# Performance work log

Measured on AMD Instinct MI355X. Metric: run time of the kernel, lower is better.

The kernel has to match this reference:

```python
import jax, jax.numpy as jnp
import numpy as np

KS = 3          # deform kernel size
N = KS * KS     # 9 sampling taps per pixel
PAD = 1         # zero padding applied before sampling (nn.ZeroPad2d)
BN_EPS = 1e-5


def conv2d(x, w, b=None, stride=1, padding=0):
    out = jax.lax.conv_general_dilated(
        x, w, (stride, stride), [(padding, padding)] * 2,
        dimension_numbers=('NCHW', 'OIHW', 'NCHW'))
    if b is not None:
        out = out + b[None, :, None, None]
    return out


def setup_inputs() -> dict:
    key = jax.random.key(0)
    ks = jax.random.split(key, 6)
    inC, outC = 128, 256
    B, H, W = 8, 64, 64

    def kaiming(k, shape):
        fan_in = shape[1] * shape[2] * shape[3]
        return jax.random.normal(k, shape, jnp.float32) / np.float32(np.sqrt(fan_in))

    return {
        'x': jax.random.normal(ks[0], (B, inC, H, W), jnp.float32),
        'w_offset': kaiming(ks[1], (2 * N, inC, 3, 3)) * 0.1,  # small offsets, realistic
        'b_offset': jnp.zeros((2 * N,), jnp.float32),
        'w_mask': kaiming(ks[2], (N, inC, 3, 3)),
        'b_mask': jnp.zeros((N,), jnp.float32),
        'w_conv': kaiming(ks[3], (outC, inC, KS, KS)),
        'bn_gamma': jnp.ones((outC,), jnp.float32),
        'bn_beta': jnp.zeros((outC,), jnp.float32),
        'bn_mean': jax.random.normal(ks[4], (outC,), jnp.float32) * 0.1,
        'bn_var': jnp.ones((outC,), jnp.float32) + jax.random.uniform(ks[5], (outC,), jnp.float32) * 0.1,
    }


def deform_conv(x, w_offset, b_offset, w_mask, b_mask, w_conv):
    B, C, H, W = x.shape
    dt = x.dtype

    offset = conv2d(x, w_offset, b_offset, 1, 1)               # (B, 2N, H, W)
    m = jax.nn.sigmoid(conv2d(x, w_mask, b_mask, 1, 1))        # (B, N, H, W)

    # kernel grid offsets p_n (first N channels = rows, last N = cols)
    rng = jnp.arange(-(KS - 1) // 2, (KS - 1) // 2 + 1, dtype=dt)
    pnx, pny = jnp.meshgrid(rng, rng, indexing='ij')
    p_n = jnp.concatenate([pnx.reshape(-1), pny.reshape(-1)])[None, :, None, None]

    # base positions p_0 (torch impl starts at 1, sampling on padded input)
    p0x = jnp.broadcast_to(jnp.arange(1, H + 1, dtype=dt)[:, None], (H, W))
    p0y = jnp.broadcast_to(jnp.arange(1, W + 1, dtype=dt)[None, :], (H, W))
    p_0 = jnp.concatenate([jnp.tile(p0x[None], (N, 1, 1)),
                           jnp.tile(p0y[None], (N, 1, 1))])[None]  # (1, 2N, H, W)

    p = (offset + p_n + p_0).transpose(0, 2, 3, 1)             # (B, H, W, 2N)

    xp = jnp.pad(x, ((0, 0), (0, 0), (PAD, PAD), (PAD, PAD)))
    Hp, Wp = H + 2 * PAD, W + 2 * PAD

    px, py = p[..., :N], p[..., N:]
    fx, fy = jnp.floor(px), jnp.floor(py)
    q_lt_x = jnp.clip(fx, 0, Hp - 1)
    q_lt_y = jnp.clip(fy, 0, Wp - 1)
    q_rb_x = jnp.clip(fx + 1, 0, Hp - 1)
    q_rb_y = jnp.clip(fy + 1, 0, Wp - 1)
    px = jnp.clip(px, 0, Hp - 1)
    py = jnp.clip(py, 0, Wp - 1)

    # bilinear weights (faithful to the reference torch formulas)
    g_lt = (1 + (q_lt_x - px)) * (1 + (q_lt_y - py))
    g_rb = (1 - (q_rb_x - px)) * (1 - (q_rb_y - py))
    g_lb = (1 + (q_lt_x - px)) * (1 - (q_rb_y - py))
    g_rt = (1 - (q_rb_x - px)) * (1 + (q_lt_y - py))

    xp_flat = xp.reshape(B, C, Hp * Wp)

    def gather(qx, qy):
        idx = (qx.astype(jnp.int32) * Wp + qy.astype(jnp.int32)).reshape(B, 1, -1)
        out = jnp.take_along_axis(xp_flat,
                                  jnp.broadcast_to(idx, (B, C, idx.shape[-1])), axis=2)
        return out.reshape(B, C, H, W, N)

    x_off = (g_lt[:, None] * gather(q_lt_x, q_lt_y)
             + g_rb[:, None] * gather(q_rb_x, q_rb_y)
             + g_lb[:, None] * gather(q_lt_x, q_rb_y)
             + g_rt[:, None] * gather(q_rb_x, q_lt_y))       # (B, C, H, W, N)

    x_off = x_off * m.transpose(0, 2, 3, 1)[:, None]          # modulation

    # (B,C,H,W,ks,ks) -> (B,C,H*ks,W*ks)  (equivalent to _reshape_x_offset)
    x_off = x_off.reshape(B, C, H, W, KS, KS).transpose(0, 1, 2, 4, 3, 5)
    x_off = x_off.reshape(B, C, H * KS, W * KS)

    return conv2d(x_off, w_conv, None, KS, 0)                 # (B, outC, H, W)


def reference(x, w_offset, b_offset, w_mask, b_mask, w_conv,
              bn_gamma, bn_beta, bn_mean, bn_var):
    y = deform_conv(x, w_offset, b_offset, w_mask, b_mask, w_conv)
    inv = jax.lax.rsqrt(bn_var + BN_EPS)
    scale = (bn_gamma * inv)[None, :, None, None]
    shift = (bn_beta - bn_mean * bn_gamma * inv)[None, :, None, None]
    return jax.nn.relu(y * scale + shift)
```

## Files before the change

kernel.cpp:

```cpp
#include <hip/hip_runtime.h>
#include <math.h>

#define BB 8
#define CC 128
#define HH 64
#define WW 64
#define NPTS 9
#define OUTC 256
#define HW (HH*WW)
#define KTOT (CC*NPTS)
#define BK 288
#define AP 290
#define WROWS 6
#define NCH 16

typedef __attribute__((ext_vector_type(8))) short bf16x8;
typedef __attribute__((ext_vector_type(4))) float f32x4;

__device__ unsigned short g_wT[OUTC * KTOT];
__device__ unsigned short g_woT[32 * KTOT];

__device__ __forceinline__ unsigned short f2bf(float f) {
    unsigned int u = __builtin_bit_cast(unsigned int, f);
    unsigned int r = (u + 0x7FFFu + ((u >> 16) & 1u)) >> 16;
    return (unsigned short)r;
}

__device__ __forceinline__ unsigned cvtpk(float lo, float hi) {
    unsigned r;
    asm("v_cvt_pk_bf16_f32 %0, %1, %2" : "=v"(r) : "v"(lo), "v"(hi));
    return r;
}
__device__ __forceinline__ float bflo(unsigned w) { return __builtin_bit_cast(float, w << 16); }
__device__ __forceinline__ float bfhi(unsigned w) { return __builtin_bit_cast(float, w & 0xFFFF0000u); }

__device__ __forceinline__ int orig_k(int k) {
    int cb = k / BK, r = k % BK;
    int pair = r / 18, r2 = r % 18;
    int n = r2 >> 1, half = r2 & 1;
    return (cb * 32 + pair * 2 + half) * NPTS + n;
}

__global__ __launch_bounds__(256) void prep_kernel(
    const float* __restrict__ wo, const float* __restrict__ wm,
    const float* __restrict__ wc)
{
    int idx = blockIdx.x * 256 + threadIdx.x;
    const int T1 = 32 * KTOT;
    if (idx < T1) {
        int nn = idx / KTOT, k = idx - nn * KTOT;
        int ok = orig_k(k);
        float v = (nn < 18) ? wo[nn * KTOT + ok]
                            : (nn < 27 ? wm[(nn - 18) * KTOT + ok] : 0.f);
        g_woT[idx] = f2bf(v);
    } else if (idx < T1 + OUTC * KTOT) {
        int j = idx - T1;
        int oc = j / KTOT, k = j - oc * KTOT;
        g_wT[j] = f2bf(wc[oc * KTOT + orig_k(k)]);
    }
}

struct PF { float a[WROWS], b[WROWS]; };

__device__ __forceinline__ void issue(PF& pf, const float* __restrict__ xb,
                                      int h, int g, int tid) {
    if (g > 15) return;
    int cb = (g >> 1) & 3, s = g & 1;
    int pair = tid >> 6, sub = tid & 63;
    const float* pA = xb + (size_t)(cb * 32 + s * NCH + pair * 2) * HW + sub;
    #pragma unroll
    for (int k = 0; k < WROWS; ++k) {
        int gr = h - 2 + k;
        bool v = (gr >= 0) & (gr < HH);
        pf.a[k] = v ? pA[gr * WW] : 0.f;
        pf.b[k] = v ? pA[HW + gr * WW] : 0.f;
    }
}

__device__ __forceinline__ void commit(unsigned* buf, const PF& pf, int tid) {
    unsigned* wp = buf + (tid >> 6) * 384 + (tid & 63);
    #pragma unroll
    for (int k = 0; k < WROWS; ++k) wp[k * 64] = cvtpk(pf.a[k], pf.b[k]);
}

__global__ __launch_bounds__(512) __attribute__((amdgpu_waves_per_eu(4, 4)))
void fused_kernel(
    const float* __restrict__ x,
    const float* __restrict__ b_offset, const float* __restrict__ b_mask,
    const float* __restrict__ bn_gamma, const float* __restrict__ bn_beta,
    const float* __restrict__ bn_mean,  const float* __restrict__ bn_var,
    float* __restrict__ out)
{
    __shared__ unsigned short Atile[64][AP];
    __shared__ unsigned win2[2][8 * 384];
    __shared__ float params[NPTS][5][64];
    float* ovf = (float*)&win2[0][0];

    int blk = blockIdx.x;
    int b = blk >> 6, h = blk & 63;
    int tid  = threadIdx.x;
    int lane = tid & 63;
    int wv   = __builtin_amdgcn_readfirstlane(tid >> 6);
    int l15  = lane & 15;
    int kg   = lane >> 4;
    int spix = lane;

    const float* xb = x + (size_t)b * CC * HW;
    unsigned* AtU = (unsigned*)&Atile[0][0];

    int mi_a = wv & 3, nf_a = wv >> 2;
    f32x4 s1acc = {0.f, 0.f, 0.f, 0.f};

    int g = 0;
    PF pf; issue(pf, xb, h, 0, tid);
    for (int cb = 0; cb < 4; ++cb) {
        for (int s = 0; s < 2; ++s) {
            commit(win2[g & 1], pf, tid);
            __syncthreads();
            issue(pf, xb, h, g + 1, tid);
            int cpair = s * 8 + wv;
            const unsigned* base = &win2[g & 1][wv * 384];
            #pragma unroll
            for (int tap = 0; tap < 9; ++tap) {
                int ky = tap / 3, kx = tap % 3;
                int col  = spix + kx - 1;
                int colc = min(max(col, 0), WW - 1);
                unsigned w = base[(ky + 1) * 64 + colc];
                w = (col >= 0 && col < WW) ? w : 0u;
                AtU[spix * 145 + cpair * 9 + tap] = w;
            }
            ++g;
        }
        __syncthreads();
        for (int q = 0; q < 9; ++q) {
            int koff = q * 32 + kg * 8;
            bf16x8 af = *(const bf16x8*)&Atile[mi_a * 16 + l15][koff];
            int nn = nf_a * 16 + l15;
            bf16x8 bfr = *(const bf16x8*)&g_woT[nn * KTOT + cb * BK + koff];
            s1acc = __builtin_amdgcn_mfma_f32_16x16x32_bf16(af, bfr, s1acc, 0, 0, 0);
        }
    }

    #pragma unroll
    for (int j = 0; j < 4; ++j) {
        float val = s1acc[j];
        int nn   = nf_a * 16 + l15;
        int pixl = mi_a * 16 + kg * 4 + j;
        if (nn < 9) {
            ovf[nn * 64 + pixl] = val + b_offset[nn] + (float)(nn / 3 - 1) + (float)(h + 1);
        } else if (nn < 18) {
            int n = nn - 9;
            ovf[576 + n * 64 + pixl] = val + b_offset[nn] + (float)(n % 3 - 1) + (float)(pixl + 1);
        } else if (nn < 27) {
            int n = nn - 18;
            float sg = val + b_mask[n];
            ovf[1152 + n * 64 + pixl] = 1.f / (1.f + expf(-sg));
        }
    }
    __syncthreads();

    if (tid < 64) {
        int t = tid;
        #pragma unroll
        for (int n = 0; n < NPTS; ++n) {
            float px = ovf[n * 64 + t];
            float py = ovf[576 + n * 64 + t];
            float m  = ovf[1152 + n * 64 + t];
            float fx = floorf(px), fy = floorf(py);
            float qltx = fminf(fmaxf(fx,       0.f), 65.f);
            float qlty = fminf(fmaxf(fy,       0.f), 65.f);
            float qrbx = fminf(fmaxf(fx + 1.f, 0.f), 65.f);
            float qrby = fminf(fmaxf(fy + 1.f, 0.f), 65.f);
            float pxc  = fminf(fmaxf(px, 0.f), 65.f);
            float pyc  = fminf(fmaxf(py, 0.f), 65.f);
            float glt = (1.f + (qltx - pxc)) * (1.f + (qlty - pyc)) * m;
            float grb = (1.f - (qrbx - pxc)) * (1.f - (qrby - pyc)) * m;
            float glb = (1.f + (qltx - pxc)) * (1.f - (qrby - pyc)) * m;
            float grt = (1.f - (qrbx - pxc)) * (1.f + (qlty - pyc)) * m;
            int i0 = (int)qltx - 1, j0 = (int)qlty - 1;
            int i1 = (int)qrbx - 1, j1 = (int)qrby - 1;
            bool v00 = (i0 >= 0) & (i0 < HH) & (j0 >= 0) & (j0 < WW);
            bool v11 = (i1 >= 0) & (i1 < HH) & (j1 >= 0) & (j1 < WW);
            bool v01 = (i0 >= 0) & (i0 < HH) & (j1 >= 0) & (j1 < WW);
            bool v10 = (i1 >= 0) & (i1 < HH) & (j0 >= 0) & (j0 < WW);
            params[n][0][t] = v00 ? glt : 0.f;
            params[n][1][t] = v11 ? grb : 0.f;
            params[n][2][t] = v01 ? glb : 0.f;
            params[n][3][t] = v10 ? grt : 0.f;
            bool okr0 = ((i0 >= h - 2) & (i0 <= h + 3)) | !(v00 | v01);
            bool okr1 = ((i1 >= h - 2) & (i1 <= h + 3)) | !(v11 | v10);
            bool ok = okr0 & okr1;
            int r0w = min(max(i0 - (h - 2), 0), WROWS - 1);
            int r1w = min(max(i1 - (h - 2), 0), WROWS - 1);
            int r0g = min(max(i0, 0), HH - 1);
            int r1g = min(max(i1, 0), HH - 1);
            int j0c = min(max(j0, 0), WW - 1);
            int j1c = min(max(j1, 0), WW - 1);
            int o  = ok ? (r0w * WW + j0c) : (r0g * WW + j0c);
            int dr = ok ? (r1w - r0w) : (r1g - r0g);
            int dj = j1c - j0c;
            unsigned pk = (unsigned)o | ((unsigned)(dr + 64) << 13)
                        | ((unsigned)(dj + 64) << 20) | ((unsigned)ok << 27);
            params[n][4][t] = __builtin_bit_cast(float, pk);
        }
    }
    __syncthreads();

    f32x4 acc[4][2];
    #pragma unroll
    for (int mi = 0; mi < 4; ++mi)
        #pragma unroll
        for (int ni = 0; ni < 2; ++ni)
            acc[mi][ni] = (f32x4){0.f, 0.f, 0.f, 0.f};

    int oc0 = wv * 32;

    for (int cb = 0; cb < 4; ++cb) {
        for (int s = 0; s < 2; ++s) {
            commit(win2[g & 1], pf, tid);
            __syncthreads();
            issue(pf, xb, h, g + 1, tid);
            int cpair = s * 8 + wv;
            const unsigned* base = &win2[g & 1][wv * 384];
            const float* xgA = xb + (size_t)(cb * 32 + s * NCH + wv * 2) * HW;
            const float* xgB = xgA + HW;
            #pragma unroll
            for (int n = 0; n < NPTS; ++n) {
                float g0 = params[n][0][spix];
                float g1 = params[n][1][spix];
                float g2 = params[n][2][spix];
                float g3 = params[n][3][spix];
                unsigned p = __builtin_bit_cast(unsigned, params[n][4][spix]);
                int o  = p & 0x1FFF;
                int d1 = ((int)((p >> 13) & 0x7F) - 64) * WW;
                int d2 = (int)((p >> 20) & 0x7F) - 64;
                float v0, v1;
                if (p & (1u << 27)) {
                    unsigned w00 = base[o];
                    unsigned w11 = base[o + d1 + d2];
                    unsigned w01 = base[o + d2];
                    unsigned w10 = base[o + d1];
                    v0 =       g0 * bflo(w00);
                    v0 = fmaf(g1, bflo(w11), v0);
                    v0 = fmaf(g2, bflo(w01), v0);
                    v0 = fmaf(g3, bflo(w10), v0);
                    v1 =       g0 * bfhi(w00);
                    v1 = fmaf(g1, bfhi(w11), v1);
                    v1 = fmaf(g2, bfhi(w01), v1);
                    v1 = fmaf(g3, bfhi(w10), v1);
                } else {
                    v0 =       g0 * xgA[o];
                    v0 = fmaf(g1, xgA[o + d1 + d2], v0);
                    v0 = fmaf(g2, xgA[o + d2], v0);
                    v0 = fmaf(g3, xgA[o + d1], v0);
                    v1 =       g0 * xgB[o];
                    v1 = fmaf(g1, xgB[o + d1 + d2], v1);
                    v1 = fmaf(g2, xgB[o + d2], v1);
                    v1 = fmaf(g3, xgB[o + d1], v1);
                }
                AtU[spix * 145 + cpair * 9 + n] = cvtpk(v0, v1);
            }
            ++g;
        }
        __syncthreads();
        for (int q = 0; q < 9; ++q) {
            int koff = q * 32 + kg * 8;
            bf16x8 af[4];
            #pragma unroll
            for (int mi = 0; mi < 4; ++mi)
                af[mi] = *(const bf16x8*)&Atile[mi * 16 + l15][koff];
            #pragma unroll
            for (int ni = 0; ni < 2; ++ni) {
                int oc = oc0 + ni * 16 + l15;
                bf16x8 bfr = *(const bf16x8*)&g_wT[oc * KTOT + cb * BK + koff];
                #pragma unroll
                for (int mi = 0; mi < 4; ++mi)
                    acc[mi][ni] = __builtin_amdgcn_mfma_f32_16x16x32_bf16(af[mi], bfr, acc[mi][ni], 0, 0, 0);
            }
        }
    }

    #pragma unroll
    for (int ni = 0; ni < 2; ++ni) {
        int oc = oc0 + ni * 16 + l15;
        float inv   = 1.f / sqrtf(bn_var[oc] + 1e-5f);
        float scale = bn_gamma[oc] * inv;
        float shift = bn_beta[oc] - bn_mean[oc] * scale;
        float* op = out + ((size_t)b * OUTC + oc) * HW + h * WW + kg * 4;
        #pragma unroll
        for (int mi = 0; mi < 4; ++mi) {
            f32x4 o4;
            #pragma unroll
            for (int j = 0; j < 4; ++j) {
                float v = fmaf(acc[mi][ni][j], scale, shift);
                o4[j] = v > 0.f ? v : 0.f;
            }
            *(f32x4*)(op + mi * 16) = o4;
        }
    }
}

extern "C" void kernel_launch(void* const* d_in, const int* in_sizes, int n_in,
                              void* d_out, int out_size, void* d_ws, size_t ws_size,
                              hipStream_t stream) {
    (void)in_sizes; (void)n_in; (void)out_size; (void)d_ws; (void)ws_size;
    const float* x        = (const float*)d_in[0];
    const float* w_offset = (const float*)d_in[1];
    const float* b_offset = (const float*)d_in[2];
    const float* w_mask   = (const float*)d_in[3];
    const float* b_mask   = (const float*)d_in[4];
    const float* w_conv   = (const float*)d_in[5];
    const float* bn_gamma = (const float*)d_in[6];
    const float* bn_beta  = (const float*)d_in[7];
    const float* bn_mean  = (const float*)d_in[8];
    const float* bn_var   = (const float*)d_in[9];
    float* out = (float*)d_out;

    int prep_elems = 32 * KTOT + OUTC * KTOT;
    prep_kernel<<<(prep_elems + 255) / 256, 256, 0, stream>>>(w_offset, w_mask, w_conv);
    fused_kernel<<<BB * HH, 512, 0, stream>>>(x, b_offset, b_mask,
                                              bn_gamma, bn_beta, bn_mean, bn_var, out);
}
```

Baseline: 93.13 us.

## Process four channels per wave per step and drop double-buffered window

The input-window staging now has each wave load four channels per chunk, packed as two bf16 pairs in a uint2, instead of two channels over two sub-steps. This halves the per-chunk staging iterations and removes the double-buffered LDS window. It also widens the bilinear gather to read a uint2 per corner and write two packed A-tile entries per tap. In exchange, a barrier is added after each MFMA block to protect the single buffer. The bf16 conversion now happens right after the global loads inside the prefetch, which may expose load latency before the MFMA section.

```diff
diff --git a/kernel.cpp b/kernel.cpp
--- a/kernel.cpp
+++ b/kernel.cpp
@@ -12,7 +12,6 @@
 #define BK 288
 #define AP 290
 #define WROWS 6
-#define NCH 16
 
 typedef __attribute__((ext_vector_type(8))) short bf16x8;
 typedef __attribute__((ext_vector_type(4))) float f32x4;
@@ -60,27 +59,31 @@
     }
 }
 
-struct PF { float a[WROWS], b[WROWS]; };
+struct PF { uint2 w[WROWS]; };
 
 __device__ __forceinline__ void issue(PF& pf, const float* __restrict__ xb,
                                       int h, int g, int tid) {
-    if (g > 15) return;
-    int cb = (g >> 1) & 3, s = g & 1;
-    int pair = tid >> 6, sub = tid & 63;
-    const float* pA = xb + (size_t)(cb * 32 + s * NCH + pair * 2) * HW + sub;
-    #pragma unroll
-    for (int k = 0; k < WROWS; ++k) {
-        int gr = h - 2 + k;
+    if (g >= 8) return;
+    int cb = g & 3;
+    int q = tid >> 6, col = tid & 63;
+    const float* base = xb + (size_t)(cb * 32 + 4 * q) * HW + col;
+    #pragma unroll
+    for (int r = 0; r < WROWS; ++r) {
+        int gr = h - 2 + r;
         bool v = (gr >= 0) & (gr < HH);
-        pf.a[k] = v ? pA[gr * WW] : 0.f;
-        pf.b[k] = v ? pA[HW + gr * WW] : 0.f;
-    }
-}
-
-__device__ __forceinline__ void commit(unsigned* buf, const PF& pf, int tid) {
-    unsigned* wp = buf + (tid >> 6) * 384 + (tid & 63);
-    #pragma unroll
-    for (int k = 0; k < WROWS; ++k) wp[k * 64] = cvtpk(pf.a[k], pf.b[k]);
+        float a0 = v ? base[0 * HW + gr * WW] : 0.f;
+        float a1 = v ? base[1 * HW + gr * WW] : 0.f;
+        float a2 = v ? base[2 * HW + gr * WW] : 0.f;
+        float a3 = v ? base[3 * HW + gr * WW] : 0.f;
+        pf.w[r].x = cvtpk(a0, a1);
+        pf.w[r].y = cvtpk(a2, a3);
+    }
+}
+
+__device__ __forceinline__ void commit(uint2* win, const PF& pf, int tid) {
+    uint2* wp = win + (tid >> 6) * 384 + (tid & 63);
+    #pragma unroll
+    for (int r = 0; r < WROWS; ++r) wp[r * 64] = pf.w[r];
 }
 
 __global__ __launch_bounds__(512) __attribute__((amdgpu_waves_per_eu(4, 4)))
@@ -92,9 +95,9 @@
     float* __restrict__ out)
 {
     __shared__ unsigned short Atile[64][AP];
-    __shared__ unsigned win2[2][8 * 384];
+    __shared__ uint2 win[8 * 384];
     __shared__ float params[NPTS][5][64];
-    float* ovf = (float*)&win2[0][0];
+    float* ovf = (float*)win;
 
     int blk = blockIdx.x;
     int b = blk >> 6, h = blk & 63;
@@ -111,26 +114,23 @@
     int mi_a = wv & 3, nf_a = wv >> 2;
     f32x4 s1acc = {0.f, 0.f, 0.f, 0.f};
 
-    int g = 0;
     PF pf; issue(pf, xb, h, 0, tid);
     for (int cb = 0; cb < 4; ++cb) {
-        for (int s = 0; s < 2; ++s) {
-            commit(win2[g & 1], pf, tid);
-            __syncthreads();
-            issue(pf, xb, h, g + 1, tid);
-            int cpair = s * 8 + wv;
-            const unsigned* base = &win2[g & 1][wv * 384];
+        commit(win, pf, tid);
+        {
+            const uint2* base = win + wv * 384;
             #pragma unroll
             for (int tap = 0; tap < 9; ++tap) {
                 int ky = tap / 3, kx = tap % 3;
                 int col  = spix + kx - 1;
                 int colc = min(max(col, 0), WW - 1);
-                unsigned w = base[(ky + 1) * 64 + colc];
-                w = (col >= 0 && col < WW) ? w : 0u;
-                AtU[spix * 145 + cpair * 9 + tap] = w;
+                uint2 v = base[(ky + 1) * 64 + colc];
+                bool cv = (col >= 0) & (col < WW);
+                AtU[spix * 145 + (2 * wv) * 9 + tap]     = cv ? v.x : 0u;
+                AtU[spix * 145 + (2 * wv + 1) * 9 + tap] = cv ? v.y : 0u;
             }
-            ++g;
-        }
+        }
+        issue(pf, xb, h, cb + 1, tid);
         __syncthreads();
         for (int q = 0; q < 9; ++q) {
             int koff = q * 32 + kg * 8;
@@ -139,6 +139,7 @@
             bf16x8 bfr = *(const bf16x8*)&g_woT[nn * KTOT + cb * BK + koff];
             s1acc = __builtin_amdgcn_mfma_f32_16x16x32_bf16(af, bfr, s1acc, 0, 0, 0);
         }
+        __syncthreads();
     }
 
     #pragma unroll
@@ -216,14 +217,10 @@
     int oc0 = wv * 32;
 
     for (int cb = 0; cb < 4; ++cb) {
-        for (int s = 0; s < 2; ++s) {
-            commit(win2[g & 1], pf, tid);
-            __syncthreads();
-            issue(pf, xb, h, g + 1, tid);
-            int cpair = s * 8 + wv;
-            const unsigned* base = &win2[g & 1][wv * 384];
-            const float* xgA = xb + (size_t)(cb * 32 + s * NCH + wv * 2) * HW;
-            const float* xgB = xgA + HW;
+        commit(win, pf, tid);
+        {
+            const uint2* baseq = win + wv * 384;
+            const float* xg = xb + (size_t)(cb * 32 + 4 * wv) * HW;
             #pragma unroll
             for (int n = 0; n < NPTS; ++n) {
                 float g0 = params[n][0][spix];
@@ -234,34 +231,43 @@
                 int o  = p & 0x1FFF;
                 int d1 = ((int)((p >> 13) & 0x7F) - 64) * WW;
                 int d2 = (int)((p >> 20) & 0x7F) - 64;
-                float v0, v1;
+                float v0, v1, v2, v3;
                 if (p & (1u << 27)) {
-                    unsigned w00 = base[o];
-                    unsigned w11 = base[o + d1 + d2];
-                    unsigned w01 = base[o + d2];
-                    unsigned w10 = base[o + d1];
-                    v0 =       g0 * bflo(w00);
-                    v0 = fmaf(g1, bflo(w11), v0);
-                    v0 = fmaf(g2, bflo(w01), v0);
-                    v0 = fmaf(g3, bflo(w10), v0);
-                    v1 =       g0 * bfhi(w00);
-                    v1 = fmaf(g1, bfhi(w11), v1);
-                    v1 = fmaf(g2, bfhi(w01), v1);
-                    v1 = fmaf(g3, bfhi(w10), v1);
+                    uint2 c00 = baseq[o];
+                    uint2 c11 = baseq[o + d1 + d2];
+                    uint2 c01 = baseq[o + d2];
+                    uint2 c10 = baseq[o + d1];
+                    v0 =       g0 * bflo(c00.x);
+                    v0 = fmaf(g1, bflo(c11.x), v0);
+                    v0 = fmaf(g2, bflo(c01.x), v0);
+                    v0 = fmaf(g3, bflo(c10.x), v0);
+                    v1 =       g0 * bfhi(c00.x);
+                    v1 = fmaf(g1, bfhi(c11.x), v1);
+                    v1 = fmaf(g2, bfhi(c01.x), v1);
+                    v1 = fmaf(g3, bfhi(c10.x), v1);
+                    v2 =       g0 * bflo(c00.y);
+                    v2 = fmaf(g1, bflo(c11.y), v2);
+                    v2 = fmaf(g2, bflo(c01.y), v2);
+                    v2 = fmaf(g3, bflo(c10.y), v2);
+                    v3 =       g0 * bfhi(c00.y);
+                    v3 = fmaf(g1, bfhi(c11.y), v3);
+                    v3 = fmaf(g2, bfhi(c01.y), v3);
+                    v3 = fmaf(g3, bfhi(c10.y), v3);
                 } else {
-                    v0 =       g0 * xgA[o];
-                    v0 = fmaf(g1, xgA[o + d1 + d2], v0);
-                    v0 = fmaf(g2, xgA[o + d2], v0);
-                    v0 = fmaf(g3, xgA[o + d1], v0);
-                    v1 =       g0 * xgB[o];
-                    v1 = fmaf(g1, xgB[o + d1 + d2], v1);
-                    v1 = fmaf(g2, xgB[o + d2], v1);
-                    v1 = fmaf(g3, xgB[o + d1], v1);
+                    const float* x0 = xg;
+                    const float* x1 = xg + HW;
+                    const float* x2 = xg + 2 * HW;
+                    const float* x3 = xg + 3 * HW;
+                    v0 = g0*x0[o]; v0 = fmaf(g1, x0[o+d1+d2], v0); v0 = fmaf(g2, x0[o+d2], v0); v0 = fmaf(g3, x0[o+d1], v0);
+                    v1 = g0*x1[o]; v1 = fmaf(g1, x1[o+d1+d2], v1); v1 = fmaf(g2, x1[o+d2], v1); v1 = fmaf(g3, x1[o+d1], v1);
+                    v2 = g0*x2[o]; v2 = fmaf(g1, x2[o+d1+d2], v2); v2 = fmaf(g2, x2[o+d2], v2); v2 = fmaf(g3, x2[o+d1], v2);
+                    v3 = g0*x3[o]; v3 = fmaf(g1, x3[o+d1+d2], v3); v3 = fmaf(g2, x3[o+d2], v3); v3 = fmaf(g3, x3[o+d1], v3);
                 }
-                AtU[spix * 145 + cpair * 9 + n] = cvtpk(v0, v1);
+                AtU[spix * 145 + (2 * wv) * 9 + n]     = cvtpk(v0, v1);
+                AtU[spix * 145 + (2 * wv + 1) * 9 + n] = cvtpk(v2, v3);
             }
-            ++g;
-        }
+        }
+        issue(pf, xb, h, 5 + cb, tid);
         __syncthreads();
         for (int q = 0; q < 9; ++q) {
             int koff = q * 32 + kg * 8;
@@ -278,6 +284,7 @@
                     acc[mi][ni] = __builtin_amdgcn_mfma_f32_16x16x32_bf16(af[mi], bfr, acc[mi][ni], 0, 0, 0);
             }
         }
+        __syncthreads();
     }
 
     #pragma unroll
```

Result: slower. 95.72 us (+2.8%).

## Use 1024-thread blocks with double-buffered A tiles and reversed second-pass channel order

Applied to the files above, without the earlier changes.

Doubles the block to 16 waves, so each wave builds one channel pair per chunk and owns 16 output channels instead of 32. The A tile is double-buffered so building the next chunk overlaps the MFMA work on the current one, which halves the barriers per chunk. The second pass walks channel blocks in reverse so the last window loaded in the first pass is reused. The prefetch now converts to bf16 at issue time, and block IDs are swizzled across batches. LDS use and register pressure rise, and only 8 of 16 waves do the offset/mask GEMM.

```diff
diff --git a/kernel.cpp b/kernel.cpp
--- a/kernel.cpp
+++ b/kernel.cpp
@@ -11,8 +11,8 @@
 #define KTOT (CC*NPTS)
 #define BK 288
 #define AP 290
+#define APW 145
 #define WROWS 6
-#define NCH 16
 
 typedef __attribute__((ext_vector_type(8))) short bf16x8;
 typedef __attribute__((ext_vector_type(4))) float f32x4;
@@ -25,7 +25,6 @@
     unsigned int r = (u + 0x7FFFu + ((u >> 16) & 1u)) >> 16;
     return (unsigned short)r;
 }
-
 __device__ __forceinline__ unsigned cvtpk(float lo, float hi) {
     unsigned r;
     asm("v_cvt_pk_bf16_f32 %0, %1, %2" : "=v"(r) : "v"(lo), "v"(hi));
@@ -60,30 +59,27 @@
     }
 }
 
-struct PF { float a[WROWS], b[WROWS]; };
+struct PF { unsigned w[WROWS]; };
 
 __device__ __forceinline__ void issue(PF& pf, const float* __restrict__ xb,
-                                      int h, int g, int tid) {
-    if (g > 15) return;
-    int cb = (g >> 1) & 3, s = g & 1;
-    int pair = tid >> 6, sub = tid & 63;
-    const float* pA = xb + (size_t)(cb * 32 + s * NCH + pair * 2) * HW + sub;
-    #pragma unroll
-    for (int k = 0; k < WROWS; ++k) {
-        int gr = h - 2 + k;
+                                      int h, int cb, int wv, int lane) {
+    const float* base = xb + (size_t)(cb * 32 + 2 * wv) * HW + lane;
+    #pragma unroll
+    for (int r = 0; r < WROWS; ++r) {
+        int gr = h - 2 + r;
         bool v = (gr >= 0) & (gr < HH);
-        pf.a[k] = v ? pA[gr * WW] : 0.f;
-        pf.b[k] = v ? pA[HW + gr * WW] : 0.f;
-    }
-}
-
-__device__ __forceinline__ void commit(unsigned* buf, const PF& pf, int tid) {
-    unsigned* wp = buf + (tid >> 6) * 384 + (tid & 63);
-    #pragma unroll
-    for (int k = 0; k < WROWS; ++k) wp[k * 64] = cvtpk(pf.a[k], pf.b[k]);
-}
-
-__global__ __launch_bounds__(512) __attribute__((amdgpu_waves_per_eu(4, 4)))
+        float a0 = v ? base[gr * WW] : 0.f;
+        float a1 = v ? base[HW + gr * WW] : 0.f;
+        pf.w[r] = cvtpk(a0, a1);
+    }
+}
+__device__ __forceinline__ void commit(unsigned* win, const PF& pf, int wv, int lane) {
+    unsigned* wp = win + wv * 384 + lane;
+    #pragma unroll
+    for (int r = 0; r < WROWS; ++r) wp[r * 64] = pf.w[r];
+}
+
+__global__ __launch_bounds__(1024) __attribute__((amdgpu_waves_per_eu(4, 4)))
 void fused_kernel(
     const float* __restrict__ x,
     const float* __restrict__ b_offset, const float* __restrict__ b_mask,
@@ -91,70 +87,126 @@
     const float* __restrict__ bn_mean,  const float* __restrict__ bn_var,
     float* __restrict__ out)
 {
-    __shared__ unsigned short Atile[64][AP];
-    __shared__ unsigned win2[2][8 * 384];
+    __shared__ unsigned short Atile[2][64][AP];
+    __shared__ unsigned win[16 * 384];
     __shared__ float params[NPTS][5][64];
-    float* ovf = (float*)&win2[0][0];
-
-    int blk = blockIdx.x;
+    __shared__ float ovf[27 * 64];
+
+    int bid = blockIdx.x;
+    int blk = (bid & 7) * 64 + (bid >> 3);
     int b = blk >> 6, h = blk & 63;
     int tid  = threadIdx.x;
     int lane = tid & 63;
     int wv   = __builtin_amdgcn_readfirstlane(tid >> 6);
     int l15  = lane & 15;
     int kg   = lane >> 4;
-    int spix = lane;
 
     const float* xb = x + (size_t)b * CC * HW;
-    unsigned* AtU = (unsigned*)&Atile[0][0];
-
-    int mi_a = wv & 3, nf_a = wv >> 2;
+    unsigned* At0 = (unsigned*)&Atile[0][0][0];
+    unsigned* At1 = (unsigned*)&Atile[1][0][0];
+
+    const unsigned* mywin = win + wv * 384;
+
+    auto buildA = [&](unsigned* AtU) {
+        #pragma unroll
+        for (int tap = 0; tap < 9; ++tap) {
+            int ky = tap / 3, kx = tap % 3;
+            int col  = lane + kx - 1;
+            int colc = min(max(col, 0), WW - 1);
+            unsigned w = mywin[(ky + 1) * 64 + colc];
+            w = (col >= 0 && col < WW) ? w : 0u;
+            AtU[lane * APW + wv * 9 + tap] = w;
+        }
+    };
+    auto buildB = [&](unsigned* AtU, int cb) {
+        const float* xgA = xb + (size_t)(cb * 32 + 2 * wv) * HW;
+        const float* xgB = xgA + HW;
+        #pragma unroll
+        for (int n = 0; n < NPTS; ++n) {
+            float g0 = params[n][0][lane];
+            float g1 = params[n][1][lane];
+            float g2 = params[n][2][lane];
+            float g3 = params[n][3][lane];
+            unsigned p = __builtin_bit_cast(unsigned, params[n][4][lane]);
+            int o  = p & 0x1FFF;
+            int d1 = ((int)((p >> 13) & 0x7F) - 64) * WW;
+            int d2 = (int)((p >> 20) & 0x7F) - 64;
+            float v0, v1;
+            if (p & (1u << 27)) {
+                unsigned w00 = mywin[o];
+                unsigned w11 = mywin[o + d1 + d2];
+                unsigned w01 = mywin[o + d2];
+                unsigned w10 = mywin[o + d1];
+                v0 =       g0 * bflo(w00);
+                v0 = fmaf(g1, bflo(w11), v0);
+                v0 = fmaf(g2, bflo(w01), v0);
+                v0 = fmaf(g3, bflo(w10), v0);
+                v1 =       g0 * bfhi(w00);
+                v1 = fmaf(g1, bfhi(w11), v1);
+                v1 = fmaf(g2, bfhi(w01), v1);
+                v1 = fmaf(g3, bfhi(w10), v1);
+            } else {
+                v0 =       g0 * xgA[o];
+                v0 = fmaf(g1, xgA[o + d1 + d2], v0);
+                v0 = fmaf(g2, xgA[o + d2], v0);
+                v0 = fmaf(g3, xgA[o + d1], v0);
+                v1 =       g0 * xgB[o];
+                v1 = fmaf(g1, xgB[o + d1 + d2], v1);
+                v1 = fmaf(g2, xgB[o + d2], v1);
+                v1 = fmaf(g3, xgB[o + d1], v1);
+            }
+            AtU[lane * APW + wv * 9 + n] = cvtpk(v0, v1);
+        }
+    };
+
+    int mi_a = wv & 3, nf_a = (wv >> 2) & 1;
     f32x4 s1acc = {0.f, 0.f, 0.f, 0.f};
-
-    int g = 0;
-    PF pf; issue(pf, xb, h, 0, tid);
+    PF pf;
+
+    issue(pf, xb, h, 0, wv, lane);
+    commit(win, pf, wv, lane);
+    buildA(At0);
+    issue(pf, xb, h, 1, wv, lane);
+    __syncthreads();
+
+    #pragma unroll
     for (int cb = 0; cb < 4; ++cb) {
-        for (int s = 0; s < 2; ++s) {
-            commit(win2[g & 1], pf, tid);
-            __syncthreads();
-            issue(pf, xb, h, g + 1, tid);
-            int cpair = s * 8 + wv;
-            const unsigned* base = &win2[g & 1][wv * 384];
-            #pragma unroll
-            for (int tap = 0; tap < 9; ++tap) {
-                int ky = tap / 3, kx = tap % 3;
-                int col  = spix + kx - 1;
-                int colc = min(max(col, 0), WW - 1);
-                unsigned w = base[(ky + 1) * 64 + colc];
-                w = (col >= 0 && col < WW) ? w : 0u;
-                AtU[spix * 145 + cpair * 9 + tap] = w;
+        unsigned* curAt  = (cb & 1) ? At1 : At0;
+        unsigned* nextAt = (cb & 1) ? At0 : At1;
+        if (cb < 3) {
+            commit(win, pf, wv, lane);
+            buildA(nextAt);
+            if (cb < 2) issue(pf, xb, h, cb + 2, wv, lane);
+        }
+        if (wv < 8) {
+            unsigned short (*Ac)[AP] = (cb & 1) ? Atile[1] : Atile[0];
+            for (int q = 0; q < 9; ++q) {
+                int koff = q * 32 + kg * 8;
+                bf16x8 af = *(const bf16x8*)&Ac[mi_a * 16 + l15][koff];
+                int nn = nf_a * 16 + l15;
+                bf16x8 bfr = *(const bf16x8*)&g_woT[nn * KTOT + cb * BK + koff];
+                s1acc = __builtin_amdgcn_mfma_f32_16x16x32_bf16(af, bfr, s1acc, 0, 0, 0);
             }
-            ++g;
         }
         __syncthreads();
-        for (int q = 0; q < 9; ++q) {
-            int koff = q * 32 + kg * 8;
-            bf16x8 af = *(const bf16x8*)&Atile[mi_a * 16 + l15][koff];
-            int nn = nf_a * 16 + l15;
-            bf16x8 bfr = *(const bf16x8*)&g_woT[nn * KTOT + cb * BK + koff];
-            s1acc = __builtin_amdgcn_mfma_f32_16x16x32_bf16(af, bfr, s1acc, 0, 0, 0);
-        }
-    }
-
-    #pragma unroll
-    for (int j = 0; j < 4; ++j) {
-        float val = s1acc[j];
-        int nn   = nf_a * 16 + l15;
-        int pixl = mi_a * 16 + kg * 4 + j;
-        if (nn < 9) {
-            ovf[nn * 64 + pixl] = val + b_offset[nn] + (float)(nn / 3 - 1) + (float)(h + 1);
-        } else if (nn < 18) {
-            int n = nn - 9;
-            ovf[576 + n * 64 + pixl] = val + b_offset[nn] + (float)(n % 3 - 1) + (float)(pixl + 1);
-        } else if (nn < 27) {
-            int n = nn - 18;
-            float sg = val + b_mask[n];
-            ovf[1152 + n * 64 + pixl] = 1.f / (1.f + expf(-sg));
+    }
+
+    if (wv < 8) {
+        #pragma unroll
+        for (int j = 0; j < 4; ++j) {
+            float val = s1acc[j];
+            int nn   = nf_a * 16 + l15;
+            int pixl = mi_a * 16 + kg * 4 + j;
+            if (nn < 9) {
+                ovf[nn * 64 + pixl] = val + b_offset[nn] + (float)(nn / 3 - 1) + (float)(h + 1);
+            } else if (nn < 18) {
+                int n = nn - 9;
+                ovf[576 + n * 64 + pixl] = val + b_offset[nn] + (float)(n % 3 - 1) + (float)(pixl + 1);
+            } else if (nn < 27) {
+                int n = nn - 18;
+                float sg = val + b_mask[n];
+                ovf[1152 + n * 64 + pixl] = 1.f / (1.f + expf(-sg));
+            }
         }
     }
     __syncthreads();
@@ -206,83 +258,42 @@
     }
     __syncthreads();
 
-    f32x4 acc[4][2];
-    #pragma unroll
-    for (int mi = 0; mi < 4; ++mi)
-        #pragma unroll
-        for (int ni = 0; ni < 2; ++ni)
-            acc[mi][ni] = (f32x4){0.f, 0.f, 0.f, 0.f};
-
-    int oc0 = wv * 32;
-
-    for (int cb = 0; cb < 4; ++cb) {
-        for (int s = 0; s < 2; ++s) {
-            commit(win2[g & 1], pf, tid);
-            __syncthreads();
-            issue(pf, xb, h, g + 1, tid);
-            int cpair = s * 8 + wv;
-            const unsigned* base = &win2[g & 1][wv * 384];
-            const float* xgA = xb + (size_t)(cb * 32 + s * NCH + wv * 2) * HW;
-            const float* xgB = xgA + HW;
-            #pragma unroll
-            for (int n = 0; n < NPTS; ++n) {
-                float g0 = params[n][0][spix];
-                float g1 = params[n][1][spix];
-                float g2 = params[n][2][spix];
-                float g3 = params[n][3][spix];
-                unsigned p = __builtin_bit_cast(unsigned, params[n][4][spix]);
-                int o  = p & 0x1FFF;
-                int d1 = ((int)((p >> 13) & 0x7F) - 64) * WW;
-                int d2 = (int)((p >> 20) & 0x7F) - 64;
-                float v0, v1;
-                if (p & (1u << 27)) {
-                    unsigned w00 = base[o];
-                    unsigned w11 = base[o + d1 + d2];
-                    unsigned w01 = base[o + d2];
-                    unsigned w10 = base[o + d1];
-                    v0 =       g0 * bflo(w00);
-                    v0 = fmaf(g1, bflo(w11), v0);
-                    v0 = fmaf(g2, bflo(w01), v0);
-                    v0 = fmaf(g3, bflo(w10), v0);
-                    v1 =       g0 * bfhi(w00);
-                    v1 = fmaf(g1, bfhi(w11), v1);
-                    v1 = fmaf(g2, bfhi(w01), v1);
-                    v1 = fmaf(g3, bfhi(w10), v1);
-                } else {
-                    v0 =       g0 * xgA[o];
-                    v0 = fmaf(g1, xgA[o + d1 + d2], v0);
-                    v0 = fmaf(g2, xgA[o + d2], v0);
-                    v0 = fmaf(g3, xgA[o + d1], v0);
-                    v1 =       g0 * xgB[o];
-                    v1 = fmaf(g1, xgB[o + d1 + d2], v1);
-                    v1 = fmaf(g2, xgB[o + d2], v1);
-                    v1 = fmaf(g3, xgB[o + d1], v1);
-                }
-                AtU[spix * 145 + cpair * 9 + n] = cvtpk(v0, v1);
-            }
-            ++g;
-        }
-        __syncthreads();
+    f32x4 acc[4];
+    #pragma unroll
+    for (int mi = 0; mi < 4; ++mi) acc[mi] = (f32x4){0.f, 0.f, 0.f, 0.f};
+    int oc0 = wv * 16;
+
+    buildB(At0, 3);
+    issue(pf, xb, h, 2, wv, lane);
+    __syncthreads();
+
+    #pragma unroll
+    for (int j = 0; j < 4; ++j) {
+        int cbm = 3 - j;
+        unsigned* nextAt = (j & 1) ? At0 : At1;
+        if (j < 3) {
+            commit(win, pf, wv, lane);
+            buildB(nextAt, 2 - j);
+            if (j < 2) issue(pf, xb, h, 1 - j, wv, lane);
+        }
+        unsigned short (*Ac)[AP] = (j & 1) ? Atile[1] : Atile[0];
         for (int q = 0; q < 9; ++q) {
             int koff = q * 32 + kg * 8;
             bf16x8 af[4];
             #pragma unroll
             for (int mi = 0; mi < 4; ++mi)
-                af[mi] = *(const bf16x8*)&Atile[mi * 16 + l15][koff];
+                af[mi] = *(const bf16x8*)&Ac[mi * 16 + l15][koff];
+            int oc = oc0 + l15;
+            bf16x8 bfr = *(const bf16x8*)&g_wT[oc * KTOT + cbm * BK + koff];
             #pragma unroll
-            for (int ni = 0; ni < 2; ++ni) {
-                int oc = oc0 + ni * 16 + l15;
-                bf16x8 bfr = *(const bf16x8*)&g_wT[oc * KTOT + cb * BK + koff];
-                #pragma unroll
-                for (int mi = 0; mi < 4; ++mi)
-                    acc[mi][ni] = __builtin_amdgcn_mfma_f32_16x16x32_bf16(af[mi], bfr, acc[mi][ni], 0, 0, 0);
-            }
-        }
-    }
-
-    #pragma unroll
-    for (int ni = 0; ni < 2; ++ni) {
-        int oc = oc0 + ni * 16 + l15;
+            for (int mi = 0; mi < 4; ++mi)
+                acc[mi] = __builtin_amdgcn_mfma_f32_16x16x32_bf16(af[mi], bfr, acc[mi], 0, 0, 0);
+        }
+        __syncthreads();
+    }
+
+    {
+        int oc = oc0 + l15;
         float inv   = 1.f / sqrtf(bn_var[oc] + 1e-5f);
         float scale = bn_gamma[oc] * inv;
         float shift = bn_beta[oc] - bn_mean[oc] * scale;
@@ -291,9 +302,9 @@
         for (int mi = 0; mi < 4; ++mi) {
             f32x4 o4;
             #pragma unroll
-            for (int j = 0; j < 4; ++j) {
-                float v = fmaf(acc[mi][ni][j], scale, shift);
-                o4[j] = v > 0.f ? v : 0.f;
+            for (int jj = 0; jj < 4; ++jj) {
+                float v = fmaf(acc[mi][jj], scale, shift);
+                o4[jj] = v > 0.f ? v : 0.f;
             }
             *(f32x4*)(op + mi * 16) = o4;
         }
@@ -318,6 +329,6 @@
 
     int prep_elems = 32 * KTOT + OUTC * KTOT;
     prep_kernel<<<(prep_elems + 255) / 256, 256, 0, stream>>>(w_offset, w_mask, w_conv);
-    fused_kernel<<<BB * HH, 512, 0, stream>>>(x, b_offset, b_mask,
-                                              bn_gamma, bn_beta, bn_mean, bn_var, out);
-}
+    fused_kernel<<<BB * HH, 1024, 0, stream>>>(x, b_offset, b_mask,
+                                               bn_gamma, bn_beta, bn_mean, bn_var, out);
+}
```

Measured after the change: 194.5 us. 109% more time.
